# Performance work log

Measured on AMD Instinct MI355X. Metric: run time of the kernel, lower is better.

## Reference

```python
import jax, jax.numpy as jnp
import numpy as np

MARGIN = 0.3
N, D = 4096, 512
NUM_CLASSES = 64

def setup_inputs() -> dict:
    key = jax.random.key(0)
    k1, k2, k3 = jax.random.split(key, 3)
    src_feat = jax.random.normal(k1, (N, D), dtype=jnp.float32)
    tgt_feat = jax.random.normal(k2, (N, D), dtype=jnp.float32)
    labels = jax.random.randint(k3, (N,), 0, NUM_CLASSES, dtype=jnp.int64)
    return {"src_feat": src_feat, "tgt_feat": tgt_feat, "labels": labels}

def reference(src_feat, tgt_feat, labels):
    # squared Euclidean distance matrix [n, n]
    e1 = jnp.sum(src_feat * src_feat, axis=1, keepdims=True)   # [n,1]
    e2 = jnp.sum(tgt_feat * tgt_feat, axis=1, keepdims=True).T  # [1,n]
    dist = e1 + e2 - 2.0 * (src_feat @ tgt_feat.T)
    dist = jnp.maximum(dist, 0.0)  # matches dist_mat[dist_mat < 0] = 0
    # same-label mask [n, n]
    mask = labels[:, None] == labels[None, :]
    # hard positive: max dist among same-label cols; hard negative: min among others
    dist_ap = jnp.max(jnp.where(mask, dist, -jnp.inf), axis=1)  # [n]
    dist_an = jnp.min(jnp.where(mask, jnp.inf, dist), axis=1)   # [n]
    # MarginRankingLoss with target y = 1: mean(relu(-(an - ap) + margin))
    loss = jnp.mean(jax.nn.relu(dist_ap - dist_an + MARGIN))
    return loss
```

## Files before the change

### kernel.cpp

```cpp
#include <hip/hip_runtime.h>
#include <hip/hip_bf16.h>
#include <stdint.h>

#define N_PTS 4096
#define DIM 512
#define MARGIN_F 0.3f
#define POS_INF_BITS 0x7f800000

typedef short bf16x8 __attribute__((ext_vector_type(8)));
typedef float f32x4 __attribute__((ext_vector_type(4)));

__device__ __forceinline__ unsigned short f2bf(float f) {
    unsigned int b = __float_as_uint(f);
    b += 0x7FFF + ((b >> 16) & 1);
    return (unsigned short)(b >> 16);
}

__device__ __forceinline__ void async16(const unsigned short* g, unsigned short* l) {
    __builtin_amdgcn_global_load_lds(
        (const __attribute__((address_space(1))) unsigned int*)g,
        (__attribute__((address_space(3))) unsigned int*)l,
        16, 0, 0);
}

#define RAW_BARRIER()  asm volatile("s_barrier" ::: "memory")
#define WAIT_VM8()     asm volatile("s_waitcnt vmcnt(8)" ::: "memory")
#define WAIT_VM0()     asm volatile("s_waitcnt vmcnt(0)" ::: "memory")

__global__ __launch_bounds__(256) void prep_kernel(
    const float* __restrict__ src, const float* __restrict__ tgt,
    unsigned short* __restrict__ src_bf, unsigned short* __restrict__ tgt_bf,
    float* __restrict__ e1, float* __restrict__ e2,
    float* __restrict__ out)
{
    const int row  = blockIdx.x * 4 + (threadIdx.x >> 6);
    const int lane = threadIdx.x & 63;

    if (blockIdx.x == 0 && threadIdx.x == 0) out[0] = 0.0f;

    const float4* s4 = (const float4*)(src + (size_t)row * DIM);
    const float4* t4 = (const float4*)(tgt + (size_t)row * DIM);
    float4 a0 = s4[lane], a1 = s4[lane + 64];
    float4 b0 = t4[lane], b1 = t4[lane + 64];

    ushort4 u;
    ushort4* so = (ushort4*)(src_bf + (size_t)row * DIM);
    ushort4* to = (ushort4*)(tgt_bf + (size_t)row * DIM);
    u.x = f2bf(a0.x); u.y = f2bf(a0.y); u.z = f2bf(a0.z); u.w = f2bf(a0.w); so[lane] = u;
    u.x = f2bf(a1.x); u.y = f2bf(a1.y); u.z = f2bf(a1.z); u.w = f2bf(a1.w); so[lane + 64] = u;
    u.x = f2bf(b0.x); u.y = f2bf(b0.y); u.z = f2bf(b0.z); u.w = f2bf(b0.w); to[lane] = u;
    u.x = f2bf(b1.x); u.y = f2bf(b1.y); u.z = f2bf(b1.z); u.w = f2bf(b1.w); to[lane + 64] = u;

    float s1 = a0.x*a0.x + a0.y*a0.y + a0.z*a0.z + a0.w*a0.w
             + a1.x*a1.x + a1.y*a1.y + a1.z*a1.z + a1.w*a1.w;
    float s2 = b0.x*b0.x + b0.y*b0.y + b0.z*b0.z + b0.w*b0.w
             + b1.x*b1.x + b1.y*b1.y + b1.z*b1.z + b1.w*b1.w;
    for (int off = 32; off; off >>= 1) {
        s1 += __shfl_down(s1, off);
        s2 += __shfl_down(s2, off);
    }
    if (lane == 0) {
        e1[row] = s1;
        e2[row] = s2;
    }
}

#define BM 256
#define BN 256
#define BK 64
#define NSTEP (DIM / BK)
#define NPART 64

__global__ __launch_bounds__(512) void dist_kernel(
    const unsigned short* __restrict__ src_bf,
    const unsigned short* __restrict__ tgt_bf,
    const float* __restrict__ e1, const float* __restrict__ e2,
    const int* __restrict__ labels,
    float* __restrict__ ap_part, float* __restrict__ an_part)
{
    __shared__ unsigned short As[2][BM * BK];
    __shared__ unsigned short Bs[2][BN * BK];
    __shared__ int   li[BM];
    __shared__ int   lj[BN];
    __shared__ float e1s[BM];
    __shared__ float e2s[BN];

    const int i0 = blockIdx.y * BM;
    const int j0 = blockIdx.x * BN;
    const int t = threadIdx.x;
    const int lane = t & 63;
    const int wave = t >> 6;

    if (t < BM) {
        li[t]  = labels[i0 + t];
        e1s[t] = e1[i0 + t];
        lj[t]  = labels[j0 + t];
        e2s[t] = e2[j0 + t];
    }

    const int srow = t >> 3;
    const int scol = (((t & 7) ^ (srow & 7))) * 8;
    const unsigned short* gA = src_bf + (size_t)(i0 + srow) * DIM + scol;
    const unsigned short* gB = tgt_bf + (size_t)(j0 + srow) * DIM + scol;
    const int dOff = wave * 512;

    const int wm = (wave >> 2) * 128;
    const int wn = (wave & 3) * 64;
    const int fr = lane & 15;
    const int quad = lane >> 4;
    const int key = fr & 7;

    f32x4 acc[8][4];
    #pragma unroll
    for (int a = 0; a < 8; a++)
        #pragma unroll
        for (int b = 0; b < 4; b++)
            acc[a][b] = (f32x4){0.f, 0.f, 0.f, 0.f};

    #pragma unroll
    for (int p = 0; p < 2; p++) {
        const int kk = p * BK;
        #pragma unroll
        for (int g = 0; g < 4; g++) {
            async16(gA + (size_t)g * 64 * DIM + kk, &As[p][0] + dOff + g * 4096);
            async16(gB + (size_t)g * 64 * DIM + kk, &Bs[p][0] + dOff + g * 4096);
        }
    }

    #pragma unroll
    for (int s = 0; s < NSTEP; s++) {
        if (s == NSTEP - 1) WAIT_VM0();
        else                WAIT_VM8();
        RAW_BARRIER();

        const unsigned short* aa = &As[s & 1][0];
        const unsigned short* bb = &Bs[s & 1][0];
        #pragma unroll
        for (int kh = 0; kh < 2; kh++) {
            const int cp = ((kh * 4 + quad) ^ key) * 8;
            bf16x8 af[8], bfv[4];
            #pragma unroll
            for (int x = 0; x < 8; x++)
                af[x] = *(const bf16x8*)&aa[(wm + x * 16 + fr) * BK + cp];
            #pragma unroll
            for (int x = 0; x < 4; x++)
                bfv[x] = *(const bf16x8*)&bb[(wn + x * 16 + fr) * BK + cp];
            #pragma unroll
            for (int tm = 0; tm < 8; tm++)
                #pragma unroll
                for (int tn = 0; tn < 4; tn++)
                    acc[tm][tn] = __builtin_amdgcn_mfma_f32_16x16x32_bf16(
                        af[tm], bfv[tn], acc[tm][tn], 0, 0, 0);
        }

        if (s + 2 < NSTEP) {
            RAW_BARRIER();
            const int kk = (s + 2) * BK;
            const int nb = s & 1;
            #pragma unroll
            for (int g = 0; g < 4; g++) {
                async16(gA + (size_t)g * 64 * DIM + kk, &As[nb][0] + dOff + g * 4096);
                async16(gB + (size_t)g * 64 * DIM + kk, &Bs[nb][0] + dOff + g * 4096);
            }
        }
    }

    const float INF = __int_as_float(POS_INF_BITS);
    const int pcol = blockIdx.x * 4 + (wave & 3);
    #pragma unroll
    for (int tm = 0; tm < 8; tm++) {
        #pragma unroll
        for (int r = 0; r < 4; r++) {
            const int rl = wm + tm * 16 + quad * 4 + r;
            const float e1v = e1s[rl];
            const int   liv = li[rl];
            float apv = 0.0f;
            float anv = INF;
            #pragma unroll
            for (int tn = 0; tn < 4; tn++) {
                const int cl = wn + tn * 16 + fr;
                float d = e1v + e2s[cl] - 2.0f * acc[tm][tn][r];
                d = fmaxf(d, 0.0f);
                if (liv == lj[cl]) apv = fmaxf(apv, d);
                else               anv = fminf(anv, d);
            }
            #pragma unroll
            for (int off = 1; off < 16; off <<= 1) {
                apv = fmaxf(apv, __shfl_xor(apv, off));
                anv = fminf(anv, __shfl_xor(anv, off));
            }
            if (fr == 0) {
                ap_part[(size_t)(i0 + rl) * NPART + pcol] = apv;
                an_part[(size_t)(i0 + rl) * NPART + pcol] = anv;
            }
        }
    }
}

__global__ __launch_bounds__(128) void loss_kernel(
    const float* __restrict__ ap_part, const float* __restrict__ an_part,
    float* __restrict__ out)
{
    const int row = blockIdx.x * 128 + threadIdx.x;
    const float4* a4 = (const float4*)(ap_part + (size_t)row * NPART);
    const float4* n4 = (const float4*)(an_part + (size_t)row * NPART);
    float apv = 0.0f;
    float anv = __int_as_float(POS_INF_BITS);
    #pragma unroll
    for (int i = 0; i < NPART / 4; i++) {
        float4 a = a4[i], n = n4[i];
        apv = fmaxf(apv, fmaxf(fmaxf(a.x, a.y), fmaxf(a.z, a.w)));
        anv = fminf(anv, fminf(fminf(n.x, n.y), fminf(n.z, n.w)));
    }
    float s = fmaxf(apv - anv + MARGIN_F, 0.0f);
    for (int off = 32; off; off >>= 1) s += __shfl_down(s, off);
    __shared__ float red[2];
    if ((threadIdx.x & 63) == 0) red[threadIdx.x >> 6] = s;
    __syncthreads();
    if (threadIdx.x == 0)
        atomicAdd(out, (red[0] + red[1]) / (float)N_PTS);
}

extern "C" void kernel_launch(void* const* d_in, const int* in_sizes, int n_in,
                              void* d_out, int out_size, void* d_ws, size_t ws_size,
                              hipStream_t stream) {
    const float* src   = (const float*)d_in[0];
    const float* tgt   = (const float*)d_in[1];
    const int* labels  = (const int*)d_in[2];

    char* ws = (char*)d_ws;
    const size_t featB = (size_t)N_PTS * DIM * sizeof(unsigned short);
    unsigned short* src_bf = (unsigned short*)ws;
    unsigned short* tgt_bf = (unsigned short*)(ws + featB);
    float* e1 = (float*)(ws + 2 * featB);
    float* e2 = e1 + N_PTS;
    float* ap_part = e2 + N_PTS;
    float* an_part = ap_part + (size_t)N_PTS * NPART;

    prep_kernel<<<N_PTS / 4, 256, 0, stream>>>(src, tgt, src_bf, tgt_bf,
                                               e1, e2, (float*)d_out);
    dim3 grid(N_PTS / BN, N_PTS / BM);
    dist_kernel<<<grid, 512, 0, stream>>>(src_bf, tgt_bf, e1, e2, labels,
                                          ap_part, an_part);
    loss_kernel<<<N_PTS / 128, 128, 0, stream>>>(ap_part, an_part, (float*)d_out);
}
```

Before: 98.26 us.

## Interleave async tile loads with MFMA phases in an 8-phase pipelined main loop

Restructures the GEMM main loop into eight phases per pair of K tiles. Each phase loads a slice of A fragments, issues part of the next tile's global-to-LDS copies, and runs a smaller MFMA block under raised wave priority. Fine-grained vmcnt waits and barriers replace the per-step double-buffer wait. The aim is to overlap memory traffic with matrix math and keep fewer fragments live in registers, at the cost of more barriers and a more delicate buffer hazard schedule.

```diff
diff --git a/kernel.cpp b/kernel.cpp
--- a/kernel.cpp
+++ b/kernel.cpp
@@ -24,7 +24,9 @@
 }
 
 #define RAW_BARRIER()  asm volatile("s_barrier" ::: "memory")
+#define WAIT_LGKM0()   asm volatile("s_waitcnt lgkmcnt(0)" ::: "memory")
 #define WAIT_VM8()     asm volatile("s_waitcnt vmcnt(8)" ::: "memory")
+#define WAIT_VM4()     asm volatile("s_waitcnt vmcnt(4)" ::: "memory")
 #define WAIT_VM0()     asm volatile("s_waitcnt vmcnt(0)" ::: "memory")
 
 __global__ __launch_bounds__(256) void prep_kernel(
@@ -68,7 +70,8 @@
 #define BM 256
 #define BN 256
 #define BK 64
-#define NSTEP (DIM / BK)
+#define NKT (DIM / BK)
+#define NIT (NKT / 2)
 #define NPART 64
 
 __global__ __launch_bounds__(512) void dist_kernel(
@@ -104,6 +107,15 @@
     const unsigned short* gB = tgt_bf + (size_t)(j0 + srow) * DIM + scol;
     const int dOff = wave * 512;
 
+#define STAGE_A(buf, kt, h) do { \
+        async16(gA + (size_t)(2*(h))   * 64 * DIM + (kt) * BK, &As[buf][0] + dOff + (2*(h))   * 4096); \
+        async16(gA + (size_t)(2*(h)+1) * 64 * DIM + (kt) * BK, &As[buf][0] + dOff + (2*(h)+1) * 4096); \
+    } while (0)
+#define STAGE_B(buf, kt, h) do { \
+        async16(gB + (size_t)(2*(h))   * 64 * DIM + (kt) * BK, &Bs[buf][0] + dOff + (2*(h))   * 4096); \
+        async16(gB + (size_t)(2*(h)+1) * 64 * DIM + (kt) * BK, &Bs[buf][0] + dOff + (2*(h)+1) * 4096); \
+    } while (0)
+
     const int wm = (wave >> 2) * 128;
     const int wn = (wave & 3) * 64;
     const int fr = lane & 15;
@@ -117,51 +129,66 @@
         for (int b = 0; b < 4; b++)
             acc[a][b] = (f32x4){0.f, 0.f, 0.f, 0.f};
 
-    #pragma unroll
-    for (int p = 0; p < 2; p++) {
-        const int kk = p * BK;
+    STAGE_A(0, 0, 0); STAGE_A(0, 0, 1);
+    STAGE_B(0, 0, 0); STAGE_B(0, 0, 1);
+    STAGE_A(1, 1, 0); STAGE_A(1, 1, 1);
+    STAGE_B(1, 1, 0); STAGE_B(1, 1, 1);
+    WAIT_VM8();
+    RAW_BARRIER();
+
+    bf16x8 bfv[4][2];
+    bf16x8 af[2][2];
+
+    #pragma unroll
+    for (int it = 0; it < NIT; ++it) {
         #pragma unroll
-        for (int g = 0; g < 4; g++) {
-            async16(gA + (size_t)g * 64 * DIM + kk, &As[p][0] + dOff + g * 4096);
-            async16(gB + (size_t)g * 64 * DIM + kk, &Bs[p][0] + dOff + g * 4096);
-        }
-    }
-
-    #pragma unroll
-    for (int s = 0; s < NSTEP; s++) {
-        if (s == NSTEP - 1) WAIT_VM0();
-        else                WAIT_VM8();
-        RAW_BARRIER();
-
-        const unsigned short* aa = &As[s & 1][0];
-        const unsigned short* bb = &Bs[s & 1][0];
-        #pragma unroll
-        for (int kh = 0; kh < 2; kh++) {
-            const int cp = ((kh * 4 + quad) ^ key) * 8;
-            bf16x8 af[8], bfv[4];
-            #pragma unroll
-            for (int x = 0; x < 8; x++)
-                af[x] = *(const bf16x8*)&aa[(wm + x * 16 + fr) * BK + cp];
-            #pragma unroll
-            for (int x = 0; x < 4; x++)
-                bfv[x] = *(const bf16x8*)&bb[(wn + x * 16 + fr) * BK + cp];
-            #pragma unroll
-            for (int tm = 0; tm < 8; tm++)
+        for (int ph = 0; ph < 8; ++ph) {
+            const int half = ph >> 2;
+            const int q = ph & 3;
+            const unsigned short* aa = &As[half][0];
+            const unsigned short* bb = &Bs[half][0];
+
+            if (q == 0) {
                 #pragma unroll
-                for (int tn = 0; tn < 4; tn++)
-                    acc[tm][tn] = __builtin_amdgcn_mfma_f32_16x16x32_bf16(
-                        af[tm], bfv[tn], acc[tm][tn], 0, 0, 0);
-        }
-
-        if (s + 2 < NSTEP) {
+                for (int x = 0; x < 4; ++x)
+                    #pragma unroll
+                    for (int kh = 0; kh < 2; ++kh)
+                        bfv[x][kh] = *(const bf16x8*)
+                            &bb[(wn + x * 16 + fr) * BK + ((kh * 4 + quad) ^ key) * 8];
+            }
+            #pragma unroll
+            for (int x = 0; x < 2; ++x)
+                #pragma unroll
+                for (int kh = 0; kh < 2; ++kh)
+                    af[x][kh] = *(const bf16x8*)
+                        &aa[(wm + (2 * q + x) * 16 + fr) * BK + ((kh * 4 + quad) ^ key) * 8];
+
+            if (ph == 0) { if (it > 0)       STAGE_A(1, 2 * it + 1, 0); }
+            if (ph == 1) { if (it > 0)       STAGE_A(1, 2 * it + 1, 1); }
+            if (ph == 2) { if (it < NIT - 1) STAGE_B(0, 2 * it + 2, 0); }
+            if (ph == 3) { if (it < NIT - 1) STAGE_B(0, 2 * it + 2, 1); }
+            if (ph == 4) { if (it < NIT - 1) STAGE_A(0, 2 * it + 2, 0); }
+            if (ph == 5) { if (it < NIT - 1) STAGE_A(0, 2 * it + 2, 1); }
+            if (ph == 6) { if (it < NIT - 1) STAGE_B(1, 2 * it + 3, 0); }
+            if (ph == 7) { if (it < NIT - 1) STAGE_B(1, 2 * it + 3, 1); }
+
             RAW_BARRIER();
-            const int kk = (s + 2) * BK;
-            const int nb = s & 1;
-            #pragma unroll
-            for (int g = 0; g < 4; g++) {
-                async16(gA + (size_t)g * 64 * DIM + kk, &As[nb][0] + dOff + g * 4096);
-                async16(gB + (size_t)g * 64 * DIM + kk, &Bs[nb][0] + dOff + g * 4096);
-            }
+            WAIT_LGKM0();
+
+            __builtin_amdgcn_s_setprio(1);
+            #pragma unroll
+            for (int x = 0; x < 2; ++x)
+                #pragma unroll
+                for (int tn = 0; tn < 4; ++tn)
+                    #pragma unroll
+                    for (int kh = 0; kh < 2; ++kh)
+                        acc[2 * q + x][tn] = __builtin_amdgcn_mfma_f32_16x16x32_bf16(
+                            af[x][kh], bfv[tn][kh], acc[2 * q + x][tn], 0, 0, 0);
+            __builtin_amdgcn_s_setprio(0);
+
+            if (ph == 3) { if (it < NIT - 1) WAIT_VM4(); else WAIT_VM0(); }
+            if (ph == 7) { if (it < NIT - 1) WAIT_VM4(); }
+            RAW_BARRIER();
         }
     }
 
@@ -195,6 +222,8 @@
             }
         }
     }
+#undef STAGE_A
+#undef STAGE_B
 }
 
 __global__ __launch_bounds__(128) void loss_kernel(
```

Measured after the change: 97.78 us. About the same (-0.5%).
